# Performance work log

Hardware: AMD Instinct MI355X
Metric: run time of the kernel (lower is better)

Reference implementation:

```python
import jax, jax.numpy as jnp
import numpy as np

N_NODES = 50000
N_EDGES = 1600000
KSIZE = 5   # kernel_size per dim
DIM = 3     # pseudo-coordinate dim


def spline_conv(x, src, dst, pseudo, W, root, bias, num_nodes):
    # Open B-spline basis, degree 1 (PyG SplineConv defaults).
    pos = pseudo * (KSIZE - 1)                         # [E, 3]
    idx = jnp.clip(jnp.floor(pos), 0, KSIZE - 2).astype(jnp.int32)
    frac = pos - idx                                   # [E, 3]
    strides = jnp.array([1, KSIZE, KSIZE * KSIZE], dtype=jnp.int32)
    x_j = x[src]                                       # [E, in]
    msg = jnp.zeros((src.shape[0], W.shape[-1]), x.dtype)
    # 2^dim = 8 active basis combinations per edge (small fixed loop).
    for b in range(2 ** DIM):
        bits = np.array([(b >> d) & 1 for d in range(DIM)])
        kidx = ((idx + jnp.asarray(bits, jnp.int32)) * strides).sum(-1)   # [E]
        basis = jnp.prod(jnp.where(jnp.asarray(bits, bool), frac, 1.0 - frac), axis=-1)  # [E]
        msg = msg + basis[:, None] * jnp.einsum('ei,eio->eo', x_j, W[kidx])
    out = jax.ops.segment_sum(msg, dst, num_segments=num_nodes)
    return out + x @ root + bias


def setup_inputs() -> dict:
    key = jax.random.key(0)
    ks = jax.random.split(key, 8)
    x = jax.random.normal(ks[0], (N_NODES, 1), jnp.float32)
    edge_index = jax.random.randint(ks[1], (2, N_EDGES), 0, N_NODES, jnp.int64)
    pseudo = jax.random.uniform(ks[2], (N_EDGES, DIM), jnp.float32)
    K = KSIZE ** DIM
    W1 = jax.random.normal(ks[3], (K, 1, 8), jnp.float32) * 0.1
    root1 = jax.random.normal(ks[4], (1, 8), jnp.float32) * 0.1
    bias1 = jnp.zeros((8,), jnp.float32)
    W2 = jax.random.normal(ks[5], (K, 8, 1), jnp.float32) * 0.1
    root2 = jax.random.normal(ks[6], (8, 1), jnp.float32) * 0.1
    bias2 = jnp.zeros((1,), jnp.float32)
    return {"x": x, "edge_index": edge_index, "pseudo": pseudo,
            "W1": W1, "root1": root1, "bias1": bias1,
            "W2": W2, "root2": root2, "bias2": bias2}


def reference(x, edge_index, pseudo, W1, root1, bias1, W2, root2, bias2):
    src = edge_index[0]
    dst = edge_index[1]
    n = x.shape[0]
    h = jax.nn.elu(spline_conv(x, src, dst, pseudo, W1, root1, bias1, n))
    out = jax.nn.elu(spline_conv(h, src, dst, pseudo, W2, root2, bias2, n))
    return out.reshape(-1)
```

## Files before the change

### kernel.cpp

```cpp
#include <hip/hip_runtime.h>
#include <hip/hip_fp16.h>
#include <math.h>

#define NK    125
#define HID   8
#define BSH   6
#define BKT   64
#define CAP   2560
#define MAXNB 1024
#define CHUNK 6272
#define PTHR  1024
#define WS    12
#define FQ    (1.f / 65536.f)

__device__ __forceinline__ float eluf(float v) {
    return v > 0.f ? v : expf(v) - 1.f;
}

__device__ __forceinline__ float dq(int q) {
    return ((float)q + 0.5f) * FQ;
}


__global__ __launch_bounds__(256) void init_cursor(int* __restrict__ cursor, int NB) {
    int b = blockIdx.x * 256 + threadIdx.x;
    if (b < NB) cursor[b] = b * CAP;
}

__global__ __launch_bounds__(PTHR) void partition_edges(
    const int* __restrict__ src, const int* __restrict__ dst,
    const float* __restrict__ pseudo,
    int* __restrict__ cursor, int2* __restrict__ pay8,
    unsigned short* __restrict__ payf2,
    int E, int NB)
{
    __shared__ int stage[CHUNK];
    __shared__ unsigned short perm[CHUNK];
    __shared__ int s_off[MAXNB + 1];
    __shared__ int s_gmo[MAXNB];

    int e0  = blockIdx.x * CHUNK;
    int cnt = min(CHUNK, E - e0);

    for (int b = threadIdx.x; b < NB; b += PTHR) s_off[b] = 0;
    __syncthreads();

    for (int i = threadIdx.x; i < cnt; i += PTHR) {
        int e = e0 + i;
        int d = dst[e];
        int b = d >> BSH;
        stage[i] = src[e] | ((d & (BKT - 1)) << 16) | (b << 22);
        atomicAdd(&s_off[b], 1);
    }
    __syncthreads();

    if (threadIdx.x < 64) {
        int per = (NB + 63) >> 6;
        int lo = threadIdx.x * per, hi = min(lo + per, NB);
        int sum = 0;
        for (int b = lo; b < hi; ++b) { int v = s_off[b]; s_off[b] = sum; sum += v; }
        int incl = sum;
        for (int d2 = 1; d2 < 64; d2 <<= 1) {
            int u = __shfl_up(incl, d2, 64);
            if ((int)threadIdx.x >= d2) incl += u;
        }
        int basep = incl - sum;
        for (int b = lo; b < hi; ++b) s_off[b] += basep;
        if (threadIdx.x == 63) s_off[NB] = incl;
    }
    __syncthreads();

    for (int b = threadIdx.x; b < NB; b += PTHR) {
        int c = s_off[b + 1] - s_off[b];
        int g = c ? atomicAdd(&cursor[b], c) : 0;
        s_gmo[b] = g - s_off[b];
    }
    __syncthreads();

    for (int i = threadIdx.x; i < cnt; i += PTHR) {
        unsigned ux = (unsigned)stage[i];
        int r = atomicAdd(&s_off[ux >> 22], 1);
        perm[r] = (unsigned short)i;
    }
    __syncthreads();

    for (int o = threadIdx.x; o < cnt; o += PTHR) {
        int i = perm[o];
        unsigned ux = (unsigned)stage[i];
        int e  = e0 + i;
        int sidx = ux & 0xFFFF;
        int nl   = (ux >> 16) & (BKT - 1);
        int b    = ux >> 22;
        float p0 = pseudo[3 * e + 0] * 4.f;
        float p1 = pseudo[3 * e + 1] * 4.f;
        float p2 = pseudo[3 * e + 2] * 4.f;
        int i0 = min(max((int)floorf(p0), 0), 3);
        int i1 = min(max((int)floorf(p1), 0), 3);
        int i2 = min(max((int)floorf(p2), 0), 3);
        float f0 = p0 - (float)i0, f1 = p1 - (float)i1, f2 = p2 - (float)i2;
        int kb = i0 + 5 * i1 + 25 * i2;
        int q0 = min((int)(f0 * 65536.f), 65535);
        int q1 = min((int)(f1 * 65536.f), 65535);
        int q2 = min((int)(f2 * 65536.f), 65535);
        int g = s_gmo[b] + o;
        if (g < (b + 1) * CAP) {
            pay8[g]  = make_int2(sidx | (kb << 16) | (nl << 23), q0 | (q1 << 16));
            payf2[g] = (unsigned short)q2;
        }
    }
}

__global__ __launch_bounds__(512) void layer1_fused(
    int2* __restrict__ pay8, unsigned short* __restrict__ payf2,
    const int* __restrict__ cursor,
    const float* __restrict__ x, const float* __restrict__ W1,
    const float* __restrict__ root1, const float* __restrict__ bias1,
    __half* __restrict__ h, int* __restrict__ ns, int* __restrict__ ne, int N)
{
    __shared__ float sW[NK * WS];
    __shared__ int2 stage[CAP];
    __shared__ unsigned short stf2[CAP];
    __shared__ unsigned short perm[CAP];
    __shared__ int hist[BKT];
    __shared__ int off[BKT + 1];
    __shared__ int cur[BKT];

    for (int i = threadIdx.x; i < NK * HID; i += 512)
        sW[(i >> 3) * WS + (i & 7)] = W1[i];
    if (threadIdx.x < BKT) hist[threadIdx.x] = 0;
    __syncthreads();

    int bkt  = blockIdx.x;
    int base = bkt * CAP;
    int cnt  = min(cursor[bkt] - base, CAP);

    for (int i = threadIdx.x; i < cnt; i += 512) {
        int2 pl = pay8[base + i];
        stage[i] = pl;
        stf2[i]  = payf2[base + i];
        atomicAdd(&hist[(pl.x >> 23) & (BKT - 1)], 1);
    }
    __syncthreads();

    if (threadIdx.x < BKT) {
        int v = hist[threadIdx.x];
        int incl = v;
        for (int d = 1; d < BKT; d <<= 1) {
            int u = __shfl_up(incl, d, 64);
            if (threadIdx.x >= d) incl += u;
        }
        off[threadIdx.x + 1] = incl;
        if (threadIdx.x == 0) off[0] = 0;
        cur[threadIdx.x] = incl - v;
    }
    __syncthreads();

    for (int i = threadIdx.x; i < cnt; i += 512) {
        int nl = (stage[i].x >> 23) & (BKT - 1);
        int pos = atomicAdd(&cur[nl], 1);
        perm[pos] = (unsigned short)i;
    }
    __syncthreads();

    for (int i = threadIdx.x; i < cnt; i += 512) {
        int pi = perm[i];
        pay8[base + i]  = stage[pi];
        payf2[base + i] = stf2[pi];
    }
    if (threadIdx.x < BKT) {
        int n = (bkt << BSH) + threadIdx.x;
        if (n < N) {
            ns[n] = base + off[threadIdx.x];
            ne[n] = base + off[threadIdx.x + 1];
        }
    }

    int nl = threadIdx.x >> 3;
    int j  = threadIdx.x & 7;
    int s = off[nl], e = off[nl + 1];

    float4 aclo = make_float4(0.f, 0.f, 0.f, 0.f);
    float4 achi = make_float4(0.f, 0.f, 0.f, 0.f);

    for (int i = s + j; i < e; i += 8) {
        int pi = perm[i];
        int2 pl = stage[pi];
        int packed = pl.x;
        float f0 = dq(pl.y & 0xFFFF);
        float f1 = dq((int)((unsigned)pl.y >> 16));
        float f2 = dq(stf2[pi]);
        int sidx = packed & 0xFFFF;
        int kb   = (packed >> 16) & 0x7F;
        float xj = x[sidx];
#pragma unroll
        for (int b = 0; b < 8; ++b) {
            int kidx = kb + (b & 1) + ((b >> 1) & 1) * 5 + ((b >> 2) & 1) * 25;
            float basis = ((b & 1) ? f0 : 1.f - f0)
                        * ((b & 2) ? f1 : 1.f - f1)
                        * ((b & 4) ? f2 : 1.f - f2);
            float w = xj * basis;
            float4 wlo = *(const float4*)&sW[kidx * WS];
            float4 whi = *(const float4*)&sW[kidx * WS + 4];
            aclo.x += w * wlo.x; aclo.y += w * wlo.y;
            aclo.z += w * wlo.z; aclo.w += w * wlo.w;
            achi.x += w * whi.x; achi.y += w * whi.y;
            achi.z += w * whi.z; achi.w += w * whi.w;
        }
    }

    float acc[HID] = {aclo.x, aclo.y, aclo.z, aclo.w, achi.x, achi.y, achi.z, achi.w};
#pragma unroll
    for (int m = 1; m < 8; m <<= 1)
#pragma unroll
        for (int o = 0; o < HID; ++o)
            acc[o] += __shfl_xor(acc[o], m, 64);

    int n = (bkt << BSH) + nl;
    if (n < N) {
        float v = acc[j] + x[n] * root1[j] + bias1[j];
        h[(size_t)n * HID + j] = __float2half(eluf(v));
    }
}

__global__ __launch_bounds__(256) void layer2_csr(
    const int2* __restrict__ pay8, const unsigned short* __restrict__ payf2,
    const int* __restrict__ ns, const int* __restrict__ ne,
    const __half* __restrict__ h, const float* __restrict__ W2,
    const float* __restrict__ root2, const float* __restrict__ bias2,
    float* __restrict__ out, int N)
{
    __shared__ float sW[NK * WS];
    for (int i = threadIdx.x; i < NK * HID; i += 256)
        sW[(i >> 3) * WS + (i & 7)] = W2[i];
    __syncthreads();

    int n = blockIdx.x * 32 + (threadIdx.x >> 3);
    int j = threadIdx.x & 7;
    int s = 0, e = 0;
    if (n < N) { s = ns[n]; e = ne[n]; }

    float msg = 0.f;
    for (int i = s + j; i < e; i += 8) {
        int2 pl = pay8[i];
        int packed = pl.x;
        float f0 = dq(pl.y & 0xFFFF);
        float f1 = dq((int)((unsigned)pl.y >> 16));
        float f2 = dq(payf2[i]);
        int sidx = packed & 0xFFFF;
        int kb   = (packed >> 16) & 0x7F;
        uint4 hw = *(const uint4*)(h + (size_t)sidx * HID);
        float2 h01 = __half22float2(*(__half2*)&hw.x);
        float2 h23 = __half22float2(*(__half2*)&hw.y);
        float2 h45 = __half22float2(*(__half2*)&hw.z);
        float2 h67 = __half22float2(*(__half2*)&hw.w);
#pragma unroll
        for (int b = 0; b < 8; ++b) {
            int kidx = kb + (b & 1) + ((b >> 1) & 1) * 5 + ((b >> 2) & 1) * 25;
            float basis = ((b & 1) ? f0 : 1.f - f0)
                        * ((b & 2) ? f1 : 1.f - f1)
                        * ((b & 4) ? f2 : 1.f - f2);
            float4 wlo = *(const float4*)&sW[kidx * WS];
            float4 whi = *(const float4*)&sW[kidx * WS + 4];
            float dot = h01.x * wlo.x + h01.y * wlo.y + h23.x * wlo.z + h23.y * wlo.w
                      + h45.x * whi.x + h45.y * whi.y + h67.x * whi.z + h67.y * whi.w;
            msg += basis * dot;
        }
    }

    if (n < N) msg += __half2float(h[(size_t)n * HID + j]) * root2[j];

#pragma unroll
    for (int m = 1; m < 8; m <<= 1)
        msg += __shfl_xor(msg, m, 64);

    if (j == 0 && n < N)
        out[n] = eluf(msg + bias2[0]);
}


__global__ __launch_bounds__(256) void spline_edge1(
    const int* __restrict__ src, const int* __restrict__ dst,
    const float* __restrict__ pseudo, const float* __restrict__ x,
    const float* __restrict__ W1, float* __restrict__ hacc, int E)
{
    __shared__ float sW[HID * NK];
    for (int i = threadIdx.x; i < HID * NK; i += blockDim.x) {
        int k = i >> 3, o = i & 7;
        sW[o * NK + k] = W1[i];
    }
    __syncthreads();
    int e = blockIdx.x * blockDim.x + threadIdx.x;
    if (e >= E) return;
    float p0 = pseudo[3 * e + 0] * 4.f, p1 = pseudo[3 * e + 1] * 4.f, p2 = pseudo[3 * e + 2] * 4.f;
    int i0 = min(max((int)floorf(p0), 0), 3);
    int i1 = min(max((int)floorf(p1), 0), 3);
    int i2 = min(max((int)floorf(p2), 0), 3);
    float f0 = p0 - i0, f1 = p1 - i1, f2 = p2 - i2;
    int kbase = i0 + 5 * i1 + 25 * i2;
    float xj = x[src[e]];
    float acc[HID];
#pragma unroll
    for (int o = 0; o < HID; ++o) acc[o] = 0.f;
#pragma unroll
    for (int b = 0; b < 8; ++b) {
        int kidx = kbase + (b & 1) + ((b >> 1) & 1) * 5 + ((b >> 2) & 1) * 25;
        float basis = ((b & 1) ? f0 : 1.f - f0) * ((b & 2) ? f1 : 1.f - f1) * ((b & 4) ? f2 : 1.f - f2);
#pragma unroll
        for (int o = 0; o < HID; ++o) acc[o] += basis * sW[o * NK + kidx];
    }
    float* hp = hacc + (size_t)dst[e] * HID;
#pragma unroll
    for (int o = 0; o < HID; ++o) atomicAdd(hp + o, xj * acc[o]);
}

__global__ __launch_bounds__(256) void node1(
    float* __restrict__ h, const float* __restrict__ x,
    const float* __restrict__ root1, const float* __restrict__ bias1, int N)
{
    int t = blockIdx.x * blockDim.x + threadIdx.x;
    if (t >= N * HID) return;
    int n = t >> 3, o = t & 7;
    h[t] = eluf(h[t] + x[n] * root1[o] + bias1[o]);
}

__global__ __launch_bounds__(256) void spline_edge2(
    const int* __restrict__ src, const int* __restrict__ dst,
    const float* __restrict__ pseudo, const float* __restrict__ h,
    const float* __restrict__ W2, float* __restrict__ oacc, int E)
{
    __shared__ float sW[HID * NK];
    for (int idx = threadIdx.x; idx < HID * NK; idx += blockDim.x) {
        int k = idx >> 3, i = idx & 7;
        sW[i * NK + k] = W2[idx];
    }
    __syncthreads();
    int e = blockIdx.x * blockDim.x + threadIdx.x;
    if (e >= E) return;
    float p0 = pseudo[3 * e + 0] * 4.f, p1 = pseudo[3 * e + 1] * 4.f, p2 = pseudo[3 * e + 2] * 4.f;
    int i0 = min(max((int)floorf(p0), 0), 3);
    int i1 = min(max((int)floorf(p1), 0), 3);
    int i2 = min(max((int)floorf(p2), 0), 3);
    float f0 = p0 - i0, f1 = p1 - i1, f2 = p2 - i2;
    int kbase = i0 + 5 * i1 + 25 * i2;
    const float4* hp4 = (const float4*)(h + (size_t)src[e] * HID);
    float4 ha = hp4[0], hb = hp4[1];
    float hj[HID] = {ha.x, ha.y, ha.z, ha.w, hb.x, hb.y, hb.z, hb.w};
    float msg = 0.f;
#pragma unroll
    for (int b = 0; b < 8; ++b) {
        int kidx = kbase + (b & 1) + ((b >> 1) & 1) * 5 + ((b >> 2) & 1) * 25;
        float basis = ((b & 1) ? f0 : 1.f - f0) * ((b & 2) ? f1 : 1.f - f1) * ((b & 4) ? f2 : 1.f - f2);
        float dot = 0.f;
#pragma unroll
        for (int i = 0; i < HID; ++i) dot += hj[i] * sW[i * NK + kidx];
        msg += basis * dot;
    }
    atomicAdd(&oacc[dst[e]], msg);
}

__global__ __launch_bounds__(256) void node2(
    const float* __restrict__ oacc, const float* __restrict__ h,
    const float* __restrict__ root2, const float* __restrict__ bias2,
    float* __restrict__ out, int N)
{
    int n = blockIdx.x * blockDim.x + threadIdx.x;
    if (n >= N) return;
    float v = oacc[n] + bias2[0];
#pragma unroll
    for (int i = 0; i < HID; ++i) v += h[(size_t)n * HID + i] * root2[i];
    out[n] = eluf(v);
}


extern "C" void kernel_launch(void* const* d_in, const int* in_sizes, int n_in,
                              void* d_out, int out_size, void* d_ws, size_t ws_size,
                              hipStream_t stream) {
    const float* x      = (const float*)d_in[0];
    const int*   ei     = (const int*)d_in[1];
    const float* pseudo = (const float*)d_in[2];
    const float* W1     = (const float*)d_in[3];
    const float* root1  = (const float*)d_in[4];
    const float* bias1  = (const float*)d_in[5];
    const float* W2     = (const float*)d_in[6];
    const float* root2  = (const float*)d_in[7];
    const float* bias2  = (const float*)d_in[8];

    int N = in_sizes[0];
    int E = in_sizes[1] / 2;
    const int* src = ei;
    const int* dst = ei + E;

    int NB = (N + BKT - 1) >> BSH;
    size_t pay8_bytes  = (size_t)NB * CAP * sizeof(int2);
    size_t payf2_bytes = (size_t)NB * CAP * sizeof(unsigned short);
    size_t h_bytes     = ((size_t)N * HID * sizeof(__half) + 15) & ~(size_t)15;
    size_t cursor_bytes = (size_t)NB * sizeof(int);
    size_t nsne_bytes  = (size_t)N * sizeof(int);
    size_t need = pay8_bytes + payf2_bytes + h_bytes + cursor_bytes + 2 * nsne_bytes + 64;

    if (NB <= MAXNB && N <= 65536 && E < (1 << 24) && ws_size >= need) {
        char* p = (char*)d_ws;
        int2*  pay8   = (int2*)p;                  p += pay8_bytes;
        unsigned short* payf2 = (unsigned short*)p; p += payf2_bytes;
        __half* h     = (__half*)p;                p += h_bytes;
        int*   cursor = (int*)p;                   p += cursor_bytes;
        int*   ns     = (int*)p;                   p += nsne_bytes;
        int*   ne     = (int*)p;

        init_cursor<<<(NB + 255) / 256, 256, 0, stream>>>(cursor, NB);
        int pblocks = (E + CHUNK - 1) / CHUNK;
        partition_edges<<<pblocks, PTHR, 0, stream>>>(src, dst, pseudo, cursor, pay8, payf2, E, NB);
        layer1_fused<<<NB, 512, 0, stream>>>(pay8, payf2, cursor, x, W1, root1, bias1, h, ns, ne, N);
        layer2_csr<<<(N + 31) / 32, 256, 0, stream>>>(pay8, payf2, ns, ne, h, W2, root2, bias2, (float*)d_out, N);
    } else {
        float* h    = (float*)d_ws;
        float* oacc = h + (size_t)N * HID;
        hipMemsetAsync(d_ws, 0, (size_t)(N * HID + N) * sizeof(float), stream);
        int eg = (E + 255) / 256;
        spline_edge1<<<eg, 256, 0, stream>>>(src, dst, pseudo, x, W1, h, E);
        node1<<<(N * HID + 255) / 256, 256, 0, stream>>>(h, x, root1, bias1, N);
        spline_edge2<<<eg, 256, 0, stream>>>(src, dst, pseudo, h, W2, oacc, E);
        node2<<<(N + 255) / 256, 256, 0, stream>>>(oacc, h, root2, bias2, (float*)d_out, N);
    }
}
```

Measured before the change: 149.8 us.

## Fuse both spline layers into one cooperative kernel with grid sync

Adds a cooperative kernel that runs layer 1, performs a grid-wide sync, then runs layer 2 reusing the per-bucket sorted edge payload already held in shared memory. This removes the second kernel launch, the re-read and re-sort of edges in layer 2, and the CSR node range arrays. The cooperative path is taken only when every bucket block fits co-resident on the device; otherwise it falls back to the old two kernels. A grid sync adds a barrier cost, and the occupancy check and attribute queries add host overhead on each call.

```diff
diff --git a/kernel.cpp b/kernel.cpp
--- a/kernel.cpp
+++ b/kernel.cpp
@@ -1,6 +1,9 @@
 #include <hip/hip_runtime.h>
 #include <hip/hip_fp16.h>
+#include <hip/hip_cooperative_groups.h>
 #include <math.h>
+
+namespace cg = cooperative_groups;
 
 #define NK    125
 #define HID   8
@@ -110,6 +113,158 @@
     }
 }
 
+__global__ __launch_bounds__(512) void layers_fused(
+    const int2* __restrict__ pay8, const unsigned short* __restrict__ payf2,
+    const int* __restrict__ cursor,
+    const float* __restrict__ x,
+    const float* __restrict__ W1, const float* __restrict__ root1,
+    const float* __restrict__ bias1,
+    const float* __restrict__ W2, const float* __restrict__ root2,
+    const float* __restrict__ bias2,
+    __half* __restrict__ h, float* __restrict__ out, int N)
+{
+    cg::grid_group grid = cg::this_grid();
+
+    __shared__ float sW[NK * WS];
+    __shared__ int2 stage[CAP];
+    __shared__ unsigned short stf2[CAP];
+    __shared__ unsigned short perm[CAP];
+    __shared__ int hist[BKT];
+    __shared__ int off[BKT + 1];
+    __shared__ int cur[BKT];
+
+    for (int i = threadIdx.x; i < NK * HID; i += 512)
+        sW[(i >> 3) * WS + (i & 7)] = W1[i];
+    if (threadIdx.x < BKT) hist[threadIdx.x] = 0;
+    __syncthreads();
+
+    int bkt  = blockIdx.x;
+    int base = bkt * CAP;
+    int cnt  = min(cursor[bkt] - base, CAP);
+
+    for (int i = threadIdx.x; i < cnt; i += 512) {
+        int2 pl = pay8[base + i];
+        stage[i] = pl;
+        stf2[i]  = payf2[base + i];
+        atomicAdd(&hist[(pl.x >> 23) & (BKT - 1)], 1);
+    }
+    __syncthreads();
+
+    if (threadIdx.x < BKT) {
+        int v = hist[threadIdx.x];
+        int incl = v;
+        for (int d = 1; d < BKT; d <<= 1) {
+            int u = __shfl_up(incl, d, 64);
+            if (threadIdx.x >= d) incl += u;
+        }
+        off[threadIdx.x + 1] = incl;
+        if (threadIdx.x == 0) off[0] = 0;
+        cur[threadIdx.x] = incl - v;
+    }
+    __syncthreads();
+
+    for (int i = threadIdx.x; i < cnt; i += 512) {
+        int nl = (stage[i].x >> 23) & (BKT - 1);
+        int pos = atomicAdd(&cur[nl], 1);
+        perm[pos] = (unsigned short)i;
+    }
+    __syncthreads();
+
+    int nl = threadIdx.x >> 3;
+    int j  = threadIdx.x & 7;
+    int s = off[nl], e = off[nl + 1];
+    int n = (bkt << BSH) + nl;
+
+    {
+        float4 aclo = make_float4(0.f, 0.f, 0.f, 0.f);
+        float4 achi = make_float4(0.f, 0.f, 0.f, 0.f);
+
+        for (int i = s + j; i < e; i += 8) {
+            int pi = perm[i];
+            int2 pl = stage[pi];
+            int packed = pl.x;
+            float f0 = dq(pl.y & 0xFFFF);
+            float f1 = dq((int)((unsigned)pl.y >> 16));
+            float f2 = dq(stf2[pi]);
+            int sidx = packed & 0xFFFF;
+            int kb   = (packed >> 16) & 0x7F;
+            float xj = x[sidx];
+#pragma unroll
+            for (int b = 0; b < 8; ++b) {
+                int kidx = kb + (b & 1) + ((b >> 1) & 1) * 5 + ((b >> 2) & 1) * 25;
+                float basis = ((b & 1) ? f0 : 1.f - f0)
+                            * ((b & 2) ? f1 : 1.f - f1)
+                            * ((b & 4) ? f2 : 1.f - f2);
+                float w = xj * basis;
+                float4 wlo = *(const float4*)&sW[kidx * WS];
+                float4 whi = *(const float4*)&sW[kidx * WS + 4];
+                aclo.x += w * wlo.x; aclo.y += w * wlo.y;
+                aclo.z += w * wlo.z; aclo.w += w * wlo.w;
+                achi.x += w * whi.x; achi.y += w * whi.y;
+                achi.z += w * whi.z; achi.w += w * whi.w;
+            }
+        }
+
+        float acc[HID] = {aclo.x, aclo.y, aclo.z, aclo.w, achi.x, achi.y, achi.z, achi.w};
+#pragma unroll
+        for (int m = 1; m < 8; m <<= 1)
+#pragma unroll
+            for (int o = 0; o < HID; ++o)
+                acc[o] += __shfl_xor(acc[o], m, 64);
+
+        if (n < N) {
+            float v = acc[j] + x[n] * root1[j] + bias1[j];
+            h[(size_t)n * HID + j] = __float2half(eluf(v));
+        }
+    }
+
+    __threadfence();
+    grid.sync();
+
+    for (int i = threadIdx.x; i < NK * HID; i += 512)
+        sW[(i >> 3) * WS + (i & 7)] = W2[i];
+    __syncthreads();
+
+    float msg = 0.f;
+    for (int i = s + j; i < e; i += 8) {
+        int pi = perm[i];
+        int2 pl = stage[pi];
+        int packed = pl.x;
+        float f0 = dq(pl.y & 0xFFFF);
+        float f1 = dq((int)((unsigned)pl.y >> 16));
+        float f2 = dq(stf2[pi]);
+        int sidx = packed & 0xFFFF;
+        int kb   = (packed >> 16) & 0x7F;
+        uint4 hw = *(const uint4*)(h + (size_t)sidx * HID);
+        float2 h01 = __half22float2(*(__half2*)&hw.x);
+        float2 h23 = __half22float2(*(__half2*)&hw.y);
+        float2 h45 = __half22float2(*(__half2*)&hw.z);
+        float2 h67 = __half22float2(*(__half2*)&hw.w);
+#pragma unroll
+        for (int b = 0; b < 8; ++b) {
+            int kidx = kb + (b & 1) + ((b >> 1) & 1) * 5 + ((b >> 2) & 1) * 25;
+            float basis = ((b & 1) ? f0 : 1.f - f0)
+                        * ((b & 2) ? f1 : 1.f - f1)
+                        * ((b & 4) ? f2 : 1.f - f2);
+            float4 wlo = *(const float4*)&sW[kidx * WS];
+            float4 whi = *(const float4*)&sW[kidx * WS + 4];
+            float dot = h01.x * wlo.x + h01.y * wlo.y + h23.x * wlo.z + h23.y * wlo.w
+                      + h45.x * whi.x + h45.y * whi.y + h67.x * whi.z + h67.y * whi.w;
+            msg += basis * dot;
+        }
+    }
+
+    if (n < N) msg += __half2float(h[(size_t)n * HID + j]) * root2[j];
+
+#pragma unroll
+    for (int m = 1; m < 8; m <<= 1)
+        msg += __shfl_xor(msg, m, 64);
+
+    if (j == 0 && n < N)
+        out[n] = eluf(msg + bias2[0]);
+}
+
+
 __global__ __launch_bounds__(512) void layer1_fused(
     int2* __restrict__ pay8, unsigned short* __restrict__ payf2,
     const int* __restrict__ cursor,
@@ -410,8 +565,26 @@
         init_cursor<<<(NB + 255) / 256, 256, 0, stream>>>(cursor, NB);
         int pblocks = (E + CHUNK - 1) / CHUNK;
         partition_edges<<<pblocks, PTHR, 0, stream>>>(src, dst, pseudo, cursor, pay8, payf2, E, NB);
-        layer1_fused<<<NB, 512, 0, stream>>>(pay8, payf2, cursor, x, W1, root1, bias1, h, ns, ne, N);
-        layer2_csr<<<(N + 31) / 32, 256, 0, stream>>>(pay8, payf2, ns, ne, h, W2, root2, bias2, (float*)d_out, N);
+
+        int coopAttr = 0, dev = 0, numCU = 0, maxb = 0;
+        hipGetDevice(&dev);
+        hipDeviceGetAttribute(&coopAttr, hipDeviceAttributeCooperativeLaunch, dev);
+        hipDeviceGetAttribute(&numCU, hipDeviceAttributeMultiprocessorCount, dev);
+        hipError_t occ = hipOccupancyMaxActiveBlocksPerMultiprocessor(
+            &maxb, (const void*)layers_fused, 512, 0);
+
+        if (coopAttr && occ == hipSuccess && (long)maxb * numCU >= NB) {
+            float* outp = (float*)d_out;
+            void* args[] = {(void*)&pay8, (void*)&payf2, (void*)&cursor,
+                            (void*)&x, (void*)&W1, (void*)&root1, (void*)&bias1,
+                            (void*)&W2, (void*)&root2, (void*)&bias2,
+                            (void*)&h, (void*)&outp, (void*)&N};
+            hipLaunchCooperativeKernel((const void*)layers_fused, dim3(NB), dim3(512),
+                                       args, 0, stream);
+        } else {
+            layer1_fused<<<NB, 512, 0, stream>>>(pay8, payf2, cursor, x, W1, root1, bias1, h, ns, ne, N);
+            layer2_csr<<<(N + 31) / 32, 256, 0, stream>>>(pay8, payf2, ns, ne, h, W2, root2, bias2, (float*)d_out, N);
+        }
     } else {
         float* h    = (float*)d_ws;
         float* oacc = h + (size_t)N * HID;
```

Measured after the change: 150.7 us. About the same (+0.6%).
